# Kernel optimization log

Measured on AMD Instinct MI355X. Metric: run time of the kernel, lower is better.

Reference implementation:

```python
import jax, jax.numpy as jnp
import numpy as np


def setup_inputs() -> dict:
    key = jax.random.key(0)
    k1, k2 = jax.random.split(key)
    D, N, M = 256, 1024, 1024
    z_x = jax.random.normal(k1, (1, D, N), dtype=jnp.float32)
    z_y = jax.random.normal(k2, (1, D, M), dtype=jnp.float32)
    return {"z_x": z_x, "z_y": z_y}


def reference(z_x, z_y):
    # squeeze().t(): (1, d, N) -> (N, d)
    x = jnp.squeeze(z_x).T  # (N, d)
    y = jnp.squeeze(z_y).T  # (M, d)
    # L1 compare: s[i, j] = -sum_d |x[i, d] - y[j, d]|  -> (N, M)
    s = -jnp.sum(jnp.abs(x[:, None, :] - y[None, :, :]), axis=-1)
    a = jax.nn.softmax(s, axis=1)  # row-wise softmax
    b = jax.nn.softmax(s, axis=0)  # column-wise softmax
    a = a + b - a * b              # soft union of alignments
    return jnp.sum(a * s) / jnp.sum(a)
```

## Files before the change

kernel.cpp:

```cpp
#include <hip/hip_runtime.h>
#include <math.h>


#define DD 256
#define NN 1024
#define NQ 256

__device__ __forceinline__ float waveMax(float v) {
  #pragma unroll
  for (int off = 32; off; off >>= 1) v = fmaxf(v, __shfl_xor(v, off, 64));
  return v;
}
__device__ __forceinline__ float waveSum(float v) {
  #pragma unroll
  for (int off = 32; off; off >>= 1) v += __shfl_xor(v, off, 64);
  return v;
}


__global__ __launch_bounds__(256, 2)
void scompute_kernel(const float* __restrict__ zx, const float* __restrict__ zy,
                     float* __restrict__ S,
                     float* __restrict__ pRM, float* __restrict__ pRL,
                     float* __restrict__ pCM, float* __restrict__ pCL) {
  const int bx = blockIdx.x;
  const int by = blockIdx.y;
  const int i0 = by * 16;
  const int t  = threadIdx.x;
  const int w  = t >> 6;
  const int ln = t & 63;

  __shared__ float xs[DD][16];
  __shared__ float ys[2][16][128];
  __shared__ float cmS[4][128];
  __shared__ float clS[4][128];

  const float4* __restrict__ X4 = (const float4*)zx;
  const float4* __restrict__ Y4 = (const float4*)zy;

  #pragma unroll
  for (int i = 0; i < 4; ++i) {
    const int k = t + i * 256;
    const int d = k >> 2, rq = k & 3;
    *(float4*)&xs[d][rq * 4] = X4[d * NQ + by * 4 + rq];
  }

  const int sd = t >> 4;
  const int sq = t & 15;
  const int jq0 = bx * 32;
  *(float4*)&ys[0][sd][sq * 4]        = Y4[sd * NQ + jq0 + sq];
  *(float4*)&ys[0][sd][(sq + 16) * 4] = Y4[sd * NQ + jq0 + sq + 16];
  __syncthreads();

  float acc[4][2];
  #pragma unroll
  for (int r = 0; r < 4; ++r) { acc[r][0] = 0.f; acc[r][1] = 0.f; }

  #pragma unroll 1
  for (int n = 0; n < DD / 16; ++n) {
    const int buf = n & 1;
    float4 p0, p1;
    if (n < DD / 16 - 1) {
      p0 = Y4[(16 * (n + 1) + sd) * NQ + jq0 + sq];
      p1 = Y4[(16 * (n + 1) + sd) * NQ + jq0 + sq + 16];
    }
    #pragma unroll
    for (int dd = 0; dd < 16; ++dd) {
      const int d = n * 16 + dd;
      const float4 xv = *(const float4*)&xs[d][w * 4];
      const float2 yv = *(const float2*)&ys[buf][dd][ln * 2];
      acc[0][0] += fabsf(xv.x - yv.x); acc[0][1] += fabsf(xv.x - yv.y);
      acc[1][0] += fabsf(xv.y - yv.x); acc[1][1] += fabsf(xv.y - yv.y);
      acc[2][0] += fabsf(xv.z - yv.x); acc[2][1] += fabsf(xv.z - yv.y);
      acc[3][0] += fabsf(xv.w - yv.x); acc[3][1] += fabsf(xv.w - yv.y);
    }
    if (n < DD / 16 - 1) {
      *(float4*)&ys[buf ^ 1][sd][sq * 4]        = p0;
      *(float4*)&ys[buf ^ 1][sd][(sq + 16) * 4] = p1;
    }
    __syncthreads();
  }

  float2* __restrict__ S2 = (float2*)S;
  #pragma unroll
  for (int r = 0; r < 4; ++r)
    S2[(i0 + w * 4 + r) * (NN / 2) + bx * 64 + ln] = make_float2(acc[r][0], acc[r][1]);

  #pragma unroll
  for (int r = 0; r < 4; ++r) {
    float m = fmaxf(-acc[r][0], -acc[r][1]);
    m = waveMax(m);
    float l = __expf(-acc[r][0] - m) + __expf(-acc[r][1] - m);
    l = waveSum(l);
    if (ln == 0) {
      pRM[bx * NN + i0 + w * 4 + r] = m;
      pRL[bx * NN + i0 + w * 4 + r] = l;
    }
  }

  #pragma unroll
  for (int c = 0; c < 2; ++c) {
    float m = fmaxf(fmaxf(-acc[0][c], -acc[1][c]), fmaxf(-acc[2][c], -acc[3][c]));
    float l = __expf(-acc[0][c] - m) + __expf(-acc[1][c] - m) +
              __expf(-acc[2][c] - m) + __expf(-acc[3][c] - m);
    cmS[w][ln * 2 + c] = m;
    clS[w][ln * 2 + c] = l;
  }
  __syncthreads();
  if (t < 128) {
    const int j = t;
    const float m0 = cmS[0][j], m1 = cmS[1][j], m2 = cmS[2][j], m3 = cmS[3][j];
    const float M = fmaxf(fmaxf(m0, m1), fmaxf(m2, m3));
    const float L = clS[0][j] * __expf(m0 - M) + clS[1][j] * __expf(m1 - M) +
                    clS[2][j] * __expf(m2 - M) + clS[3][j] * __expf(m3 - M);
    pCM[by * NN + bx * 128 + j] = M;
    pCL[by * NN + bx * 128 + j] = L;
  }
}

__global__ __launch_bounds__(256)
void combine_kernel(const float* __restrict__ pRM, const float* __restrict__ pRL,
                    const float* __restrict__ pCM, const float* __restrict__ pCL,
                    float* __restrict__ rmax, float* __restrict__ rsum,
                    float* __restrict__ cmax, float* __restrict__ csum,
                    float* __restrict__ accum) {
  const int b = blockIdx.x, t = threadIdx.x;
  if (b == 0 && t == 0) {
    accum[0] = 0.f; accum[1] = 0.f; ((unsigned int*)accum)[2] = 0u;
  }
  if (b < 16) {
    __shared__ float sm[4][64], sl[4][64];
    const int c = t & 63;
    const int g = t >> 6;
    const int j = b * 64 + c;
    float m = -1e30f;
    #pragma unroll
    for (int k = 0; k < 16; ++k) m = fmaxf(m, pCM[(g * 16 + k) * NN + j]);
    float l = 0.f;
    #pragma unroll
    for (int k = 0; k < 16; ++k)
      l += __expf(pCM[(g * 16 + k) * NN + j] - m) * pCL[(g * 16 + k) * NN + j];
    sm[g][c] = m; sl[g][c] = l;
    __syncthreads();
    if (g == 0) {
      const float m0 = sm[0][c], m1 = sm[1][c], m2 = sm[2][c], m3 = sm[3][c];
      const float M = fmaxf(fmaxf(m0, m1), fmaxf(m2, m3));
      const float L = sl[0][c] * __expf(m0 - M) + sl[1][c] * __expf(m1 - M) +
                      sl[2][c] * __expf(m2 - M) + sl[3][c] * __expf(m3 - M);
      cmax[j] = M; csum[j] = L;
    }
  } else {
    const int r = (b - 16) * 256 + t;
    float mk[8], lk[8];
    #pragma unroll
    for (int k = 0; k < 8; ++k) { mk[k] = pRM[k * NN + r]; lk[k] = pRL[k * NN + r]; }
    float m = mk[0];
    #pragma unroll
    for (int k = 1; k < 8; ++k) m = fmaxf(m, mk[k]);
    float l = 0.f;
    #pragma unroll
    for (int k = 0; k < 8; ++k) l += lk[k] * __expf(mk[k] - m);
    rmax[r] = m; rsum[r] = l;
  }
}

__global__ __launch_bounds__(256)
void final_kernel(const float* __restrict__ S,
                  const float* __restrict__ rmax, const float* __restrict__ rsum,
                  const float* __restrict__ cmax, const float* __restrict__ csum,
                  float* __restrict__ accum, float* __restrict__ out) {
  __shared__ float redn[4], redd[4];
  const int t = threadIdx.x;
  const int row0 = blockIdx.x * 2;
  const float4* S4 = (const float4*)S;
  const float4 cm = ((const float4*)cmax)[t];
  const float4 cs = ((const float4*)csum)[t];
  float un = 0.f, ud = 0.f;
  #pragma unroll
  for (int r = 0; r < 2; ++r) {
    const int row = row0 + r;
    const float rm = rmax[row];
    const float ri = 1.f / rsum[row];
    const float4 p = S4[row * NQ + t];
    {
      const float s = -p.x;
      const float a = __expf(s - rm) * ri;
      const float b = __expf(s - cm.x) / cs.x;
      const float u = a + b - a * b;
      un += u * s; ud += u;
    }
    {
      const float s = -p.y;
      const float a = __expf(s - rm) * ri;
      const float b = __expf(s - cm.y) / cs.y;
      const float u = a + b - a * b;
      un += u * s; ud += u;
    }
    {
      const float s = -p.z;
      const float a = __expf(s - rm) * ri;
      const float b = __expf(s - cm.z) / cs.z;
      const float u = a + b - a * b;
      un += u * s; ud += u;
    }
    {
      const float s = -p.w;
      const float a = __expf(s - rm) * ri;
      const float b = __expf(s - cm.w) / cs.w;
      const float u = a + b - a * b;
      un += u * s; ud += u;
    }
  }
  un = waveSum(un); ud = waveSum(ud);
  if ((t & 63) == 0) { redn[t >> 6] = un; redd[t >> 6] = ud; }
  __syncthreads();
  if (t == 0) {
    atomicAdd(&accum[0], redn[0] + redn[1] + redn[2] + redn[3]);
    atomicAdd(&accum[1], redd[0] + redd[1] + redd[2] + redd[3]);
    __threadfence();
    unsigned int* cnt = (unsigned int*)accum + 2;
    const unsigned int old = atomicAdd(cnt, 1u);
    if (old == gridDim.x - 1) {
      const float n = atomicAdd(&accum[0], 0.f);
      const float d = atomicAdd(&accum[1], 0.f);
      out[0] = n / d;
    }
  }
}


#define TJ  128
#define NCH (NN / TJ)
#define BLK 256

__global__ __launch_bounds__(BLK)
void stats2_kernel(const float* __restrict__ zx, const float* __restrict__ zy,
                   float* __restrict__ partM, float* __restrict__ partS) {
  const int side = blockIdx.z;
  const float* __restrict__ X = side ? zy : zx;
  const float* __restrict__ Y = side ? zx : zy;
  const int j0 = blockIdx.x * TJ;
  const int i0 = blockIdx.y * 8;
  const int t  = threadIdx.x;
  const int rg = t >> 5;
  const int c  = t & 31;

  __shared__ float xs[8 * DD];
  for (int k = t; k < 8 * DD; k += BLK)
    xs[k] = X[(k >> 3) * NN + i0 + (k & 7)];
  __syncthreads();

  const float4* __restrict__ Y4 = (const float4*)Y;
  const int yb = (j0 >> 2) + c;
  float4 acc = make_float4(0.f, 0.f, 0.f, 0.f);
  #pragma unroll 8
  for (int d = 0; d < DD; ++d) {
    const float4 yv = Y4[d * NQ + yb];
    const float xv = xs[d * 8 + rg];
    acc.x += fabsf(xv - yv.x);
    acc.y += fabsf(xv - yv.y);
    acc.z += fabsf(xv - yv.z);
    acc.w += fabsf(xv - yv.w);
  }

  float m = fmaxf(fmaxf(-acc.x, -acc.y), fmaxf(-acc.z, -acc.w));
  #pragma unroll
  for (int off = 16; off > 0; off >>= 1) m = fmaxf(m, __shfl_xor(m, off, 32));
  float p = __expf(-acc.x - m) + __expf(-acc.y - m) +
            __expf(-acc.z - m) + __expf(-acc.w - m);
  #pragma unroll
  for (int off = 16; off > 0; off >>= 1) p += __shfl_xor(p, off, 32);

  if (c == 0) {
    const int idx = side * (NCH * NN) + blockIdx.x * NN + (i0 + rg);
    partM[idx] = m;
    partS[idx] = p;
  }
}

__global__ __launch_bounds__(BLK)
void combine_kernel_fb(const float* __restrict__ partM, const float* __restrict__ partS,
                       float* __restrict__ rmax, float* __restrict__ rsum,
                       float* __restrict__ cmax, float* __restrict__ csum,
                       float* __restrict__ accum) {
  const int gid = blockIdx.x * BLK + threadIdx.x;
  if (gid == 0) { accum[0] = 0.f; accum[1] = 0.f; }
  const int sd = gid >> 10;
  const int i  = gid & (NN - 1);
  float mk[NCH], sk[NCH];
  #pragma unroll
  for (int k = 0; k < NCH; ++k) {
    mk[k] = partM[sd * (NCH * NN) + k * NN + i];
    sk[k] = partS[sd * (NCH * NN) + k * NN + i];
  }
  float m = mk[0];
  #pragma unroll
  for (int k = 1; k < NCH; ++k) m = fmaxf(m, mk[k]);
  float s = 0.f;
  #pragma unroll
  for (int k = 0; k < NCH; ++k) s += __expf(mk[k] - m) * sk[k];
  if (sd == 0) { rmax[i] = m; rsum[i] = s; }
  else         { cmax[i] = m; csum[i] = s; }
}

__global__ __launch_bounds__(BLK)
void final2_kernel(const float* __restrict__ zx, const float* __restrict__ zy,
                   const float* __restrict__ rmax, const float* __restrict__ rsum,
                   const float* __restrict__ cmax, const float* __restrict__ csum,
                   float* __restrict__ accum) {
  const int j0 = blockIdx.x * TJ;
  const int i0 = blockIdx.y * 8;
  const int t  = threadIdx.x;
  const int rg = t >> 5;
  const int c  = t & 31;

  __shared__ float xs[8 * DD];
  __shared__ float redn[4], redd[4];
  for (int k = t; k < 8 * DD; k += BLK)
    xs[k] = zx[(k >> 3) * NN + i0 + (k & 7)];
  __syncthreads();

  const float4* __restrict__ Y4 = (const float4*)zy;
  const int yb = (j0 >> 2) + c;
  float4 acc = make_float4(0.f, 0.f, 0.f, 0.f);
  #pragma unroll 8
  for (int d = 0; d < DD; ++d) {
    const float4 yv = Y4[d * NQ + yb];
    const float xv = xs[d * 8 + rg];
    acc.x += fabsf(xv - yv.x);
    acc.y += fabsf(xv - yv.y);
    acc.z += fabsf(xv - yv.z);
    acc.w += fabsf(xv - yv.w);
  }

  const int i = i0 + rg;
  const float rm = rmax[i];
  const float ri = 1.f / rsum[i];
  const float4 cm = ((const float4*)cmax)[yb];
  const float4 cs = ((const float4*)csum)[yb];

  float un = 0.f, ud = 0.f;
  {
    const float s = -acc.x;
    const float a = __expf(s - rm) * ri;
    const float b = __expf(s - cm.x) / cs.x;
    const float u = a + b - a * b;
    un += u * s; ud += u;
  }
  {
    const float s = -acc.y;
    const float a = __expf(s - rm) * ri;
    const float b = __expf(s - cm.y) / cs.y;
    const float u = a + b - a * b;
    un += u * s; ud += u;
  }
  {
    const float s = -acc.z;
    const float a = __expf(s - rm) * ri;
    const float b = __expf(s - cm.z) / cs.z;
    const float u = a + b - a * b;
    un += u * s; ud += u;
  }
  {
    const float s = -acc.w;
    const float a = __expf(s - rm) * ri;
    const float b = __expf(s - cm.w) / cs.w;
    const float u = a + b - a * b;
    un += u * s; ud += u;
  }

  un = waveSum(un); ud = waveSum(ud);
  if ((t & 63) == 0) { redn[t >> 6] = un; redd[t >> 6] = ud; }
  __syncthreads();
  if (t == 0) {
    atomicAdd(&accum[0], redn[0] + redn[1] + redn[2] + redn[3]);
    atomicAdd(&accum[1], redd[0] + redd[1] + redd[2] + redd[3]);
  }
}

__global__ void finalize_kernel(const float* __restrict__ accum, float* __restrict__ out) {
  out[0] = accum[0] / accum[1];
}


extern "C" void kernel_launch(void* const* d_in, const int* in_sizes, int n_in,
                              void* d_out, int out_size, void* d_ws, size_t ws_size,
                              hipStream_t stream) {
  const float* zx = (const float*)d_in[0];
  const float* zy = (const float*)d_in[1];
  float* ws  = (float*)d_ws;
  float* out = (float*)d_out;

  float* accum = ws;
  float* S     = ws + 16;
  float* pRM   = S + NN * NN;
  float* pRL   = pRM + 8 * NN;
  float* pCM   = pRL + 8 * NN;
  float* pCL   = pCM + 64 * NN;
  float* rmax  = pCL + 64 * NN;
  float* rsum  = rmax + NN;
  float* cmax  = rsum + NN;
  float* csum  = cmax + NN;
  const size_t need = (size_t)((csum + NN) - ws) * sizeof(float);

  if (ws_size >= need) {
    dim3 g1(8, 64);
    scompute_kernel<<<g1, 256, 0, stream>>>(zx, zy, S, pRM, pRL, pCM, pCL);
    combine_kernel<<<20, 256, 0, stream>>>(pRM, pRL, pCM, pCL,
                                           rmax, rsum, cmax, csum, accum);
    final_kernel<<<NN / 2, 256, 0, stream>>>(S, rmax, rsum, cmax, csum, accum, out);
  } else {
    float* partM = ws + 16;
    float* partS = partM + 2 * NCH * NN;
    float* frmax = partS + 2 * NCH * NN;
    float* frsum = frmax + NN;
    float* fcmax = frsum + NN;
    float* fcsum = fcmax + NN;
    dim3 sgrid(NCH, NN / 8, 2);
    stats2_kernel<<<sgrid, BLK, 0, stream>>>(zx, zy, partM, partS);
    combine_kernel_fb<<<(2 * NN) / BLK, BLK, 0, stream>>>(partM, partS,
                                                          frmax, frsum, fcmax, fcsum, accum);
    dim3 fgrid(NCH, NN / 8);
    final2_kernel<<<fgrid, BLK, 0, stream>>>(zx, zy, frmax, frsum, fcmax, fcsum, accum);
    finalize_kernel<<<1, 1, 0, stream>>>(accum, out);
  }
}
```

Before: 105.5 us.

## Fuse three kernels into one cooperative kernel, keep scores in registers

Merges the score, combine and final passes into a single cooperative launch of 512 blocks that uses grid.sync between phases. Each thread keeps its L1-distance accumulators in registers across the syncs, so the 4 MB score matrix is never written to or read back from global memory. This removes two launches and the round-trip of the score matrix. In exchange it adds two grid-wide barriers, idles most blocks during the small combine phase, and needs all 512 blocks to be co-resident, which the launch bounds of 2 blocks per CU on 256 CUs allow.

```diff
diff --git a/kernel.cpp b/kernel.cpp
--- a/kernel.cpp
+++ b/kernel.cpp
@@ -1,5 +1,8 @@
 #include <hip/hip_runtime.h>
+#include <hip/hip_cooperative_groups.h>
 #include <math.h>
+
+namespace cg = cooperative_groups;
 
 
 #define DD 256
@@ -19,22 +22,30 @@
 
 
 __global__ __launch_bounds__(256, 2)
-void scompute_kernel(const float* __restrict__ zx, const float* __restrict__ zy,
-                     float* __restrict__ S,
-                     float* __restrict__ pRM, float* __restrict__ pRL,
-                     float* __restrict__ pCM, float* __restrict__ pCL) {
-  const int bx = blockIdx.x;
-  const int by = blockIdx.y;
-  const int i0 = by * 16;
-  const int t  = threadIdx.x;
-  const int w  = t >> 6;
-  const int ln = t & 63;
+void fused_kernel(const float* __restrict__ zx, const float* __restrict__ zy,
+                  float* __restrict__ pRM, float* __restrict__ pRL,
+                  float* __restrict__ pCM, float* __restrict__ pCL,
+                  float* __restrict__ rmax, float* __restrict__ rsum,
+                  float* __restrict__ cmax, float* __restrict__ csum,
+                  float* __restrict__ accum, float* __restrict__ out) {
+  cg::grid_group grid = cg::this_grid();
+  const int bid = blockIdx.x;
+  const int bx  = bid & 7;
+  const int by  = bid >> 3;
+  const int i0  = by * 16;
+  const int t   = threadIdx.x;
+  const int w   = t >> 6;
+  const int ln  = t & 63;
 
   __shared__ float xs[DD][16];
   __shared__ float ys[2][16][128];
   __shared__ float cmS[4][128];
   __shared__ float clS[4][128];
 
+  if (bid == 0 && t == 0) {
+    accum[0] = 0.f; accum[1] = 0.f; ((unsigned int*)accum)[2] = 0u;
+  }
+
   const float4* __restrict__ X4 = (const float4*)zx;
   const float4* __restrict__ Y4 = (const float4*)zy;
 
@@ -44,7 +55,6 @@
     const int d = k >> 2, rq = k & 3;
     *(float4*)&xs[d][rq * 4] = X4[d * NQ + by * 4 + rq];
   }
-
   const int sd = t >> 4;
   const int sq = t & 15;
   const int jq0 = bx * 32;
@@ -81,11 +91,6 @@
     __syncthreads();
   }
 
-  float2* __restrict__ S2 = (float2*)S;
-  #pragma unroll
-  for (int r = 0; r < 4; ++r)
-    S2[(i0 + w * 4 + r) * (NN / 2) + bx * 64 + ln] = make_float2(acc[r][0], acc[r][1]);
-
   #pragma unroll
   for (int r = 0; r < 4; ++r) {
     float m = fmaxf(-acc[r][0], -acc[r][1]);
@@ -116,23 +121,14 @@
     pCM[by * NN + bx * 128 + j] = M;
     pCL[by * NN + bx * 128 + j] = L;
   }
-}
-
-__global__ __launch_bounds__(256)
-void combine_kernel(const float* __restrict__ pRM, const float* __restrict__ pRL,
-                    const float* __restrict__ pCM, const float* __restrict__ pCL,
-                    float* __restrict__ rmax, float* __restrict__ rsum,
-                    float* __restrict__ cmax, float* __restrict__ csum,
-                    float* __restrict__ accum) {
-  const int b = blockIdx.x, t = threadIdx.x;
-  if (b == 0 && t == 0) {
-    accum[0] = 0.f; accum[1] = 0.f; ((unsigned int*)accum)[2] = 0u;
-  }
-  if (b < 16) {
-    __shared__ float sm[4][64], sl[4][64];
+
+  grid.sync();
+
+  if (bid < 16) {
+    __syncthreads();
     const int c = t & 63;
     const int g = t >> 6;
-    const int j = b * 64 + c;
+    const int j = bid * 64 + c;
     float m = -1e30f;
     #pragma unroll
     for (int k = 0; k < 16; ++k) m = fmaxf(m, pCM[(g * 16 + k) * NN + j]);
@@ -140,17 +136,17 @@
     #pragma unroll
     for (int k = 0; k < 16; ++k)
       l += __expf(pCM[(g * 16 + k) * NN + j] - m) * pCL[(g * 16 + k) * NN + j];
-    sm[g][c] = m; sl[g][c] = l;
+    cmS[g][c] = m; clS[g][c] = l;
     __syncthreads();
     if (g == 0) {
-      const float m0 = sm[0][c], m1 = sm[1][c], m2 = sm[2][c], m3 = sm[3][c];
+      const float m0 = cmS[0][c], m1 = cmS[1][c], m2 = cmS[2][c], m3 = cmS[3][c];
       const float M = fmaxf(fmaxf(m0, m1), fmaxf(m2, m3));
-      const float L = sl[0][c] * __expf(m0 - M) + sl[1][c] * __expf(m1 - M) +
-                      sl[2][c] * __expf(m2 - M) + sl[3][c] * __expf(m3 - M);
+      const float L = clS[0][c] * __expf(m0 - M) + clS[1][c] * __expf(m1 - M) +
+                      clS[2][c] * __expf(m2 - M) + clS[3][c] * __expf(m3 - M);
       cmax[j] = M; csum[j] = L;
     }
-  } else {
-    const int r = (b - 16) * 256 + t;
+  } else if (bid < 20) {
+    const int r = (bid - 16) * 256 + t;
     float mk[8], lk[8];
     #pragma unroll
     for (int k = 0; k < 8; ++k) { mk[k] = pRM[k * NN + r]; lk[k] = pRL[k * NN + r]; }
@@ -162,61 +158,39 @@
     for (int k = 0; k < 8; ++k) l += lk[k] * __expf(mk[k] - m);
     rmax[r] = m; rsum[r] = l;
   }
-}
-
-__global__ __launch_bounds__(256)
-void final_kernel(const float* __restrict__ S,
-                  const float* __restrict__ rmax, const float* __restrict__ rsum,
-                  const float* __restrict__ cmax, const float* __restrict__ csum,
-                  float* __restrict__ accum, float* __restrict__ out) {
-  __shared__ float redn[4], redd[4];
-  const int t = threadIdx.x;
-  const int row0 = blockIdx.x * 2;
-  const float4* S4 = (const float4*)S;
-  const float4 cm = ((const float4*)cmax)[t];
-  const float4 cs = ((const float4*)csum)[t];
+
+  grid.sync();
+
+  const float2 cmv = ((const float2*)cmax)[bx * 64 + ln];
+  const float2 csv = ((const float2*)csum)[bx * 64 + ln];
   float un = 0.f, ud = 0.f;
   #pragma unroll
-  for (int r = 0; r < 2; ++r) {
-    const int row = row0 + r;
+  for (int r = 0; r < 4; ++r) {
+    const int row = i0 + w * 4 + r;
     const float rm = rmax[row];
     const float ri = 1.f / rsum[row];
-    const float4 p = S4[row * NQ + t];
     {
-      const float s = -p.x;
+      const float s = -acc[r][0];
       const float a = __expf(s - rm) * ri;
-      const float b = __expf(s - cm.x) / cs.x;
+      const float b = __expf(s - cmv.x) / csv.x;
       const float u = a + b - a * b;
       un += u * s; ud += u;
     }
     {
-      const float s = -p.y;
+      const float s = -acc[r][1];
       const float a = __expf(s - rm) * ri;
-      const float b = __expf(s - cm.y) / cs.y;
+      const float b = __expf(s - cmv.y) / csv.y;
       const float u = a + b - a * b;
       un += u * s; ud += u;
     }
-    {
-      const float s = -p.z;
-      const float a = __expf(s - rm) * ri;
-      const float b = __expf(s - cm.z) / cs.z;
-      const float u = a + b - a * b;
-      un += u * s; ud += u;
-    }
-    {
-      const float s = -p.w;
-      const float a = __expf(s - rm) * ri;
-      const float b = __expf(s - cm.w) / cs.w;
-      const float u = a + b - a * b;
-      un += u * s; ud += u;
-    }
   }
   un = waveSum(un); ud = waveSum(ud);
-  if ((t & 63) == 0) { redn[t >> 6] = un; redd[t >> 6] = ud; }
+  __syncthreads();
+  if (ln == 0) { cmS[0][w] = un; clS[0][w] = ud; }
   __syncthreads();
   if (t == 0) {
-    atomicAdd(&accum[0], redn[0] + redn[1] + redn[2] + redn[3]);
-    atomicAdd(&accum[1], redd[0] + redd[1] + redd[2] + redd[3]);
+    atomicAdd(&accum[0], cmS[0][0] + cmS[0][1] + cmS[0][2] + cmS[0][3]);
+    atomicAdd(&accum[1], clS[0][0] + clS[0][1] + clS[0][2] + clS[0][3]);
     __threadfence();
     unsigned int* cnt = (unsigned int*)accum + 2;
     const unsigned int old = atomicAdd(cnt, 1u);
@@ -392,8 +366,7 @@
   float* out = (float*)d_out;
 
   float* accum = ws;
-  float* S     = ws + 16;
-  float* pRM   = S + NN * NN;
+  float* pRM   = ws + 16;
   float* pRL   = pRM + 8 * NN;
   float* pCM   = pRL + 8 * NN;
   float* pCL   = pCM + 64 * NN;
@@ -404,11 +377,14 @@
   const size_t need = (size_t)((csum + NN) - ws) * sizeof(float);
 
   if (ws_size >= need) {
-    dim3 g1(8, 64);
-    scompute_kernel<<<g1, 256, 0, stream>>>(zx, zy, S, pRM, pRL, pCM, pCL);
-    combine_kernel<<<20, 256, 0, stream>>>(pRM, pRL, pCM, pCL,
-                                           rmax, rsum, cmax, csum, accum);
-    final_kernel<<<NN / 2, 256, 0, stream>>>(S, rmax, rsum, cmax, csum, accum, out);
+    void* args[] = {
+      (void*)&zx, (void*)&zy,
+      (void*)&pRM, (void*)&pRL, (void*)&pCM, (void*)&pCL,
+      (void*)&rmax, (void*)&rsum, (void*)&cmax, (void*)&csum,
+      (void*)&accum, (void*)&out
+    };
+    hipLaunchCooperativeKernel((void*)fused_kernel, dim3(512), dim3(256),
+                               args, 0, stream);
   } else {
     float* partM = ws + 16;
     float* partS = partM + 2 * NCH * NN;
```

Result: slower. 203.2 us (+92.6%).
